# Kernel optimization log

Measured on AMD Instinct MI355X. Metric: run time of the kernel, lower is better.

The kernel has to match this reference:

```python
import jax, jax.numpy as jnp
import numpy as np

N_HEADS = 16

def setup_inputs() -> dict:
    key = jax.random.key(0)
    k1, k2, k3 = jax.random.split(key, 3)
    B, L, D = 2, 2048, 1024
    x = jax.random.normal(k1, (B, L, D), dtype=jnp.float32)
    w_qkv = jax.random.normal(k2, (D, 3 * D), dtype=jnp.float32) * (D ** -0.5)
    w_proj = jax.random.normal(k3, (D, D), dtype=jnp.float32) * (D ** -0.5)
    return {"x": x, "w_qkv": w_qkv, "w_proj": w_proj}

def reference(x, w_qkv, w_proj):
    B, L, D = x.shape
    H = N_HEADS
    dh = D // H
    qkv = x @ w_qkv  # [B,L,3D]
    q, k, v = jnp.split(qkv, 3, axis=-1)
    def heads(t):
        return t.reshape(B, L, H, dh).transpose(0, 2, 1, 3)  # [B,H,L,dh]
    q, k, v = heads(q), heads(k), heads(v)
    s = jnp.einsum('bhqd,bhkd->bhqk', q, k) / jnp.sqrt(jnp.float32(dh))
    causal = jnp.tril(jnp.ones((L, L), dtype=bool))
    s = jnp.where(causal[None, None], s, jnp.float32(-jnp.inf))
    w = jax.nn.softmax(s, axis=-1)
    o = jnp.einsum('bhqk,bhkd->bhqd', w, v)  # [B,H,L,dh]
    o = o.transpose(0, 2, 1, 3).reshape(B, L, D)
    return o @ w_proj
```

## Files before the change

kernel.cpp:

```cpp
#include <hip/hip_runtime.h>
#include <hip/hip_bf16.h>
#include <cstddef>

typedef __attribute__((ext_vector_type(8))) short bf16x8;
typedef __attribute__((ext_vector_type(4))) float f32x4;
typedef __attribute__((ext_vector_type(4))) unsigned short us4;
typedef __attribute__((ext_vector_type(8))) unsigned short us8;
typedef unsigned short u16;
typedef unsigned int u32;

__device__ __forceinline__ u16 f2bf(float f) {
    unsigned u = __builtin_bit_cast(unsigned, f);
    u += 0x7FFFu + ((u >> 16) & 1u);
    return (u16)(u >> 16);
}
__device__ __forceinline__ float bf2f(u16 h) {
    unsigned u = ((unsigned)h) << 16;
    return __builtin_bit_cast(float, u);
}

__device__ __forceinline__ void gl_lds16(const u16* g, u16* l) {
    __builtin_amdgcn_global_load_lds(
        (const __attribute__((address_space(1))) u32*)g,
        (__attribute__((address_space(3))) u32*)l, 16, 0, 0);
}

template <int N>
__device__ __forceinline__ void wait_vmcnt() {
    if constexpr (N == 8)      asm volatile("s_waitcnt vmcnt(8)" ::: "memory");
    else if constexpr (N == 6) asm volatile("s_waitcnt vmcnt(6)" ::: "memory");
    else                       asm volatile("s_waitcnt vmcnt(0)" ::: "memory");
}

__global__ __launch_bounds__(256) void split_rm(const float* __restrict__ in,
                                                u16* __restrict__ hi,
                                                u16* __restrict__ lo, int n4) {
    int i = blockIdx.x * 256 + threadIdx.x;
    const int stride = gridDim.x * 256;
    for (; i < n4; i += stride) {
        f32x4 v = ((const f32x4*)in)[i];
        us4 h, l;
#pragma unroll
        for (int e = 0; e < 4; ++e) {
            u16 hb = f2bf(v[e]);
            h[e] = hb;
            l[e] = f2bf(v[e] - bf2f(hb));
        }
        ((us4*)hi)[i] = h;
        ((us4*)lo)[i] = l;
    }
}

__global__ __launch_bounds__(256) void split_T(const float* __restrict__ in, int inRS,
                                               u16* __restrict__ oh,
                                               u16* __restrict__ ol, int outRS) {
    __shared__ u16 Th[64][68], Tl[64][68];
    const int tid = threadIdx.x;
    const int sr = tid >> 4;
    const int sc = (tid & 15) * 4;
    const size_t r0 = (size_t)blockIdx.y * 64;
    const size_t c0 = (size_t)blockIdx.x * 64;

#pragma unroll
    for (int i = 0; i < 4; ++i) {
        int r = sr + i * 16;
        f32x4 v = *(const f32x4*)(in + (r0 + r) * inRS + c0 + sc);
#pragma unroll
        for (int e = 0; e < 4; ++e) {
            u16 hb = f2bf(v[e]);
            Th[sc + e][r] = hb;
            Tl[sc + e][r] = f2bf(v[e] - bf2f(hb));
        }
    }
    __syncthreads();
#pragma unroll
    for (int i = 0; i < 4; ++i) {
        int r = sr + i * 16;
        *(us4*)&oh[(c0 + r) * outRS + r0 + sc] = *(const us4*)&Th[r][sc];
        *(us4*)&ol[(c0 + r) * outRS + r0 + sc] = *(const us4*)&Tl[r][sc];
    }
}

template <int BN>
__global__ __launch_bounds__(256, 2) void gemm_bf2(
    const u16* __restrict__ Ah_g, const u16* __restrict__ Al_g,
    const u16* __restrict__ Bh_g, const u16* __restrict__ Bl_g,
    int N, int K, int gy, int mode,
    float* __restrict__ Cf,
    u16* __restrict__ qsh, u16* __restrict__ qsl,
    u16* __restrict__ ksh, u16* __restrict__ ksl,
    float* __restrict__ vtmp) {
    constexpr int NB    = BN / 32;
    constexpr int ASZ   = 128 * 32;
    constexpr int BSZ   = BN * 32;
    constexpr int SET   = 2 * ASZ + 2 * BSZ;
    constexpr int BCALL = BN / 64;
    constexpr int NCALL = 4 + 2 * BCALL;
    __shared__ u16 LB[2 * SET];

    const int tid  = threadIdx.x;
    const int lane = tid & 63;
    const int w    = tid >> 6;

    const int nwg = gridDim.x;
    const int swz = (blockIdx.x & 7) * (nwg >> 3) + (blockIdx.x >> 3);
    const int bm = (swz % gy) * 128;
    const int bn = (swz / gy) * BN;

    const int srow = lane >> 2;
    const int c_l  = (lane & 3) ^ ((lane >> 3) & 3);

    const u16* pA[2][2];
    const u16* pB[2][BCALL];
#pragma unroll
    for (int j = 0; j < 2; ++j) {
        const size_t r = (size_t)(bm + w * 32 + j * 16 + srow);
        pA[0][j] = Ah_g + r * K + c_l * 8;
        pA[1][j] = Al_g + r * K + c_l * 8;
    }
#pragma unroll
    for (int j = 0; j < BCALL; ++j) {
        const size_t r = (size_t)(bn + w * (BN / 4) + j * 16 + srow);
        pB[0][j] = Bh_g + r * K + c_l * 8;
        pB[1][j] = Bl_g + r * K + c_l * 8;
    }

    auto stage = [&](int buf, int kt) {
        u16* s = LB + buf * SET;
        const size_t ko = (size_t)kt * 32;
#pragma unroll
        for (int p = 0; p < 2; ++p)
#pragma unroll
            for (int j = 0; j < 2; ++j)
                gl_lds16(pA[p][j] + ko, s + p * ASZ + (w * 32 + j * 16) * 32);
#pragma unroll
        for (int p = 0; p < 2; ++p)
#pragma unroll
            for (int j = 0; j < BCALL; ++j)
                gl_lds16(pB[p][j] + ko,
                         s + 2 * ASZ + p * BSZ + (w * (BN / 4) + j * 16) * 32);
    };

    const int lr = lane & 15;
    const int lg = lane >> 4;
    const int wm = (w >> 1) * 64;
    const int wn = (w & 1) * (BN / 2);
    const int fc = (lg ^ ((lr >> 1) & 3)) * 8;

    f32x4 acc[4][NB] = {};

    const int NK = K >> 5;
    stage(0, 0);
    if (NK > 1) stage(1, 1);

    for (int kt = 0; kt < NK; ++kt) {
        const int cur = kt & 1;
        if (kt + 1 < NK) wait_vmcnt<NCALL>();
        else             wait_vmcnt<0>();
        __builtin_amdgcn_s_barrier();

        const u16* s = LB + cur * SET;
        bf16x8 fah[4], fal[4], fbh[NB], fbl[NB];
#pragma unroll
        for (int m = 0; m < 4; ++m) {
            const int ro = (wm + m * 16 + lr) * 32 + fc;
            fah[m] = __builtin_bit_cast(bf16x8, *(const us8*)(s + ro));
            fal[m] = __builtin_bit_cast(bf16x8, *(const us8*)(s + ASZ + ro));
        }
#pragma unroll
        for (int n = 0; n < NB; ++n) {
            const int ro = (wn + n * 16 + lr) * 32 + fc;
            fbh[n] = __builtin_bit_cast(bf16x8, *(const us8*)(s + 2 * ASZ + ro));
            fbl[n] = __builtin_bit_cast(bf16x8, *(const us8*)(s + 2 * ASZ + BSZ + ro));
        }
#pragma unroll
        for (int m = 0; m < 4; ++m)
#pragma unroll
            for (int n = 0; n < NB; ++n) {
                acc[m][n] = __builtin_amdgcn_mfma_f32_16x16x32_bf16(fah[m], fbh[n], acc[m][n], 0, 0, 0);
                acc[m][n] = __builtin_amdgcn_mfma_f32_16x16x32_bf16(fah[m], fbl[n], acc[m][n], 0, 0, 0);
                acc[m][n] = __builtin_amdgcn_mfma_f32_16x16x32_bf16(fal[m], fbh[n], acc[m][n], 0, 0, 0);
            }

        asm volatile("s_waitcnt lgkmcnt(0)" ::: "memory");
        __builtin_amdgcn_s_barrier();
        if (kt + 2 < NK) stage(cur, kt + 2);
    }

    const int orow = bm + wm + lg * 4;
    if (mode == 0) {
        const int ocol = bn + wn + lr;
#pragma unroll
        for (int m = 0; m < 4; ++m)
#pragma unroll
            for (int r = 0; r < 4; ++r) {
                const size_t row = (size_t)(orow + m * 16 + r);
#pragma unroll
                for (int n = 0; n < NB; ++n)
                    Cf[row * N + ocol + n * 16] = acc[m][n][r];
            }
    } else {
        const int sec = bn >> 10;
        const int cbase = (bn & 1023) + wn + lr;
#pragma unroll
        for (int m = 0; m < 4; ++m)
#pragma unroll
            for (int r = 0; r < 4; ++r) {
                const size_t row = (size_t)(orow + m * 16 + r);
#pragma unroll
                for (int n = 0; n < NB; ++n) {
                    float v = acc[m][n][r];
                    const size_t idx = row * 1024 + cbase + n * 16;
                    if (sec == 0) {
                        v *= 0.125f;
                        u16 hb = f2bf(v);
                        qsh[idx] = hb;
                        qsl[idx] = f2bf(v - bf2f(hb));
                    } else if (sec == 1) {
                        u16 hb = f2bf(v);
                        ksh[idx] = hb;
                        ksl[idx] = f2bf(v - bf2f(hb));
                    } else {
                        vtmp[idx] = v;
                    }
                }
            }
    }
}

__global__ __launch_bounds__(512, 4) void attn_v2(
    const u16* __restrict__ qsh, const u16* __restrict__ qsl,
    const u16* __restrict__ ksh, const u16* __restrict__ ksl,
    const u16* __restrict__ vth, const u16* __restrict__ vtl,
    u16* __restrict__ oh, u16* __restrict__ ol) {
    __shared__ u16 KH[4096], KL[4096], VH[4096], VL[4096];
    __shared__ u16 Ph[128][72], Pl[128][72];

    const int tid  = threadIdx.x;
    const int lane = tid & 63;
    const int w    = tid >> 6;
    const int wq0  = w * 16;
    const int lr   = lane & 15;
    const int lg   = lane >> 4;

    const int bid  = blockIdx.x;
    const int half = bid >> 8;
    const int idx  = bid & 255;
    const int bh   = idx & 31;
    const int jj   = idx >> 5;
    const int qt   = half ? jj : (15 - jj);
    const int b    = bh >> 4;
    const int h    = bh & 15;
    const int NT   = 2 * qt + 2;
    const size_t tokb = (size_t)b * 2048;

    const size_t qtok = tokb + (size_t)qt * 128 + wq0 + lr;
    const u16* qph = qsh + qtok * 1024 + h * 64 + lg * 8;
    const u16* qpl = qsl + qtok * 1024 + h * 64 + lg * 8;
    bf16x8 aqh[2], aql[2];
    aqh[0] = __builtin_bit_cast(bf16x8, *(const us8*)qph);
    aqh[1] = __builtin_bit_cast(bf16x8, *(const us8*)(qph + 32));
    aql[0] = __builtin_bit_cast(bf16x8, *(const us8*)qpl);
    aql[1] = __builtin_bit_cast(bf16x8, *(const us8*)(qpl + 32));

    const int rl    = lane >> 3;
    const int rbase = w * 8;
    const int cl    = (lane & 7) ^ rl;
    const u16* kh0 = ksh + (tokb + rbase + rl) * 1024 + h * 64 + cl * 8;
    const u16* kl0 = ksl + (tokb + rbase + rl) * 1024 + h * 64 + cl * 8;
    const u16* vh0 = vth + (size_t)(h * 64 + rbase + rl) * 4096 + tokb + cl * 8;
    const u16* vl0 = vtl + (size_t)(h * 64 + rbase + rl) * 4096 + tokb + cl * 8;
    u16* ldsKH = KH + rbase * 64;
    u16* ldsKL = KL + rbase * 64;
    u16* ldsVH = VH + rbase * 64;
    u16* ldsVL = VL + rbase * 64;

    gl_lds16(kh0, ldsKH);
    gl_lds16(kl0, ldsKL);
    gl_lds16(vh0, ldsVH);
    gl_lds16(vl0, ldsVL);

    float m_i[4], l_i[4];
    f32x4 acc_o[4] = {};
#pragma unroll
    for (int r = 0; r < 4; ++r) { m_i[r] = -1e30f; l_i[r] = 0.f; }

    for (int kt = 0; kt < NT; ++kt) {
        const int koff = kt * 64 - qt * 128;
        const bool active = !(kt == NT - 1 && wq0 < 64);

        asm volatile("s_waitcnt vmcnt(2)" ::: "memory");
        __builtin_amdgcn_s_barrier();

        f32x4 accs[4] = {};
        if (active) {
#pragma unroll
            for (int ks = 0; ks < 2; ++ks) {
                bf16x8 a0 = aqh[ks], a1 = aql[ks];
#pragma unroll
                for (int n = 0; n < 4; ++n) {
                    const int row = n * 16 + lr;
                    const u16* pk = KH + row * 64 + (((ks * 4 + lg) ^ (row & 7)) << 3);
                    bf16x8 bkh = __builtin_bit_cast(bf16x8, *(const us8*)pk);
                    bf16x8 bkl = __builtin_bit_cast(bf16x8, *(const us8*)(pk + 4096));
                    accs[n] = __builtin_amdgcn_mfma_f32_16x16x32_bf16(a0, bkh, accs[n], 0, 0, 0);
                    accs[n] = __builtin_amdgcn_mfma_f32_16x16x32_bf16(a0, bkl, accs[n], 0, 0, 0);
                    accs[n] = __builtin_amdgcn_mfma_f32_16x16x32_bf16(a1, bkh, accs[n], 0, 0, 0);
                }
            }
            if (koff + 63 > wq0) {
#pragma unroll
                for (int n = 0; n < 4; ++n)
#pragma unroll
                    for (int rr = 0; rr < 4; ++rr)
                        if (koff + n * 16 + lr > wq0 + 4 * lg + rr)
                            accs[n][rr] = -1e30f;
            }
#pragma unroll
            for (int rr = 0; rr < 4; ++rr) {
                float pm = fmaxf(fmaxf(accs[0][rr], accs[1][rr]),
                                 fmaxf(accs[2][rr], accs[3][rr]));
#pragma unroll
                for (int off = 1; off < 16; off <<= 1)
                    pm = fmaxf(pm, __shfl_xor(pm, off));
                float mnew  = fmaxf(m_i[rr], pm);
                float alpha = __expf(m_i[rr] - mnew);
                float ps = 0.f;
                const int prow = wq0 + 4 * lg + rr;
#pragma unroll
                for (int n = 0; n < 4; ++n) {
                    float p = __expf(accs[n][rr] - mnew);
                    u16 phb = f2bf(p);
                    Ph[prow][n * 16 + lr] = phb;
                    Pl[prow][n * 16 + lr] = f2bf(p - bf2f(phb));
                    ps += p;
                }
#pragma unroll
                for (int off = 1; off < 16; off <<= 1)
                    ps += __shfl_xor(ps, off);
                l_i[rr] = l_i[rr] * alpha + ps;
                m_i[rr] = mnew;
#pragma unroll
                for (int n = 0; n < 4; ++n) acc_o[n][rr] *= alpha;
            }
        }

        asm volatile("s_waitcnt vmcnt(0)" ::: "memory");
        asm volatile("s_waitcnt lgkmcnt(0)" ::: "memory");
        __builtin_amdgcn_s_barrier();

        if (kt + 1 < NT) {
            gl_lds16(kh0 + (size_t)(kt + 1) * 65536, ldsKH);
            gl_lds16(kl0 + (size_t)(kt + 1) * 65536, ldsKL);
        }

        if (active) {
#pragma unroll
            for (int ks = 0; ks < 2; ++ks) {
                bf16x8 aph = __builtin_bit_cast(bf16x8, *(const us8*)&Ph[wq0 + lr][ks * 32 + lg * 8]);
                bf16x8 apl = __builtin_bit_cast(bf16x8, *(const us8*)&Pl[wq0 + lr][ks * 32 + lg * 8]);
#pragma unroll
                for (int n = 0; n < 4; ++n) {
                    const int row = n * 16 + lr;
                    const u16* pv = VH + row * 64 + (((ks * 4 + lg) ^ (row & 7)) << 3);
                    bf16x8 bvh = __builtin_bit_cast(bf16x8, *(const us8*)pv);
                    bf16x8 bvl = __builtin_bit_cast(bf16x8, *(const us8*)(pv + 4096));
                    acc_o[n] = __builtin_amdgcn_mfma_f32_16x16x32_bf16(aph, bvh, acc_o[n], 0, 0, 0);
                    acc_o[n] = __builtin_amdgcn_mfma_f32_16x16x32_bf16(aph, bvl, acc_o[n], 0, 0, 0);
                    acc_o[n] = __builtin_amdgcn_mfma_f32_16x16x32_bf16(apl, bvh, acc_o[n], 0, 0, 0);
                }
            }
        }

        asm volatile("s_waitcnt lgkmcnt(0)" ::: "memory");
        __builtin_amdgcn_s_barrier();

        if (kt + 1 < NT) {
            gl_lds16(vh0 + (kt + 1) * 64, ldsVH);
            gl_lds16(vl0 + (kt + 1) * 64, ldsVL);
        }
    }

#pragma unroll
    for (int rr = 0; rr < 4; ++rr) {
        float inv = 1.0f / l_i[rr];
        const size_t q = (size_t)qt * 128 + wq0 + 4 * lg + rr;
#pragma unroll
        for (int n = 0; n < 4; ++n) {
            float v = acc_o[n][rr] * inv;
            const size_t oidx = (tokb + q) * 1024 + h * 64 + n * 16 + lr;
            u16 hb = f2bf(v);
            oh[oidx] = hb;
            ol[oidx] = f2bf(v - bf2f(hb));
        }
    }
}

extern "C" void kernel_launch(void* const* d_in, const int* in_sizes, int n_in,
                              void* d_out, int out_size, void* d_ws, size_t ws_size,
                              hipStream_t stream) {
    const float* x      = (const float*)d_in[0];
    const float* w_qkv  = (const float*)d_in[1];
    const float* w_proj = (const float*)d_in[2];
    float* out = (float*)d_out;

    char* ws = (char*)d_ws;
    const size_t MB = 1u << 20;
    u16* wqkvT_h  = (u16*)(ws + 0 * MB);
    u16* wqkvT_l  = (u16*)(ws + 6 * MB);
    u16* wprojT_h = (u16*)(ws + 12 * MB);
    u16* wprojT_l = (u16*)(ws + 14 * MB);
    u16* xh       = (u16*)(ws + 16 * MB);
    u16* xl       = (u16*)(ws + 24 * MB);
    u16* qsh      = (u16*)(ws + 32 * MB);
    u16* qsl      = (u16*)(ws + 40 * MB);
    u16* ksh      = (u16*)(ws + 48 * MB);
    u16* ksl      = (u16*)(ws + 56 * MB);
    float* vtmp   = (float*)(ws + 64 * MB);
    u16* vth = xh;
    u16* vtl = xl;
    u16* oh = (u16*)vtmp;
    u16* ol = oh + (size_t)4096 * 1024;

    split_rm<<<2048, 256, 0, stream>>>(x, xh, xl, 4096 * 1024 / 4);
    split_T<<<dim3(48, 16), 256, 0, stream>>>(w_qkv, 3072, wqkvT_h, wqkvT_l, 1024);
    split_T<<<dim3(16, 16), 256, 0, stream>>>(w_proj, 1024, wprojT_h, wprojT_l, 1024);

    gemm_bf2<128><<<dim3(768), 256, 0, stream>>>(xh, xl, wqkvT_h, wqkvT_l,
                                                 3072, 1024, 32, 1,
                                                 nullptr, qsh, qsl, ksh, ksl, vtmp);

    split_T<<<dim3(16, 64), 256, 0, stream>>>(vtmp, 1024, vth, vtl, 4096);

    attn_v2<<<dim3(512), 512, 0, stream>>>(qsh, qsl, ksh, ksl, vth, vtl, oh, ol);

    gemm_bf2<64><<<dim3(512), 256, 0, stream>>>(oh, ol, wprojT_h, wprojT_l,
                                                1024, 1024, 32, 0,
                                                out, nullptr, nullptr, nullptr, nullptr, nullptr);
}
```

Baseline: 322.6 us.

## Fuse input split kernels, widen QKV GEMM tile, remap block swizzle

Merges the three fp32-to-bf16 hi/lo split launches (x, w_qkv, w_proj) into a single prep kernel dispatched on block index, removing two launches. The QKV GEMM moves from a 128-wide to a 192-wide N tile, cutting the grid from 768 to 512 blocks, and its epilogue now derives the Q/K/V section per column because a 192-wide tile can straddle section boundaries. Block-to-tile mapping becomes a parameterised grouped swizzle (RM/RBM/RBN) aimed at L2 reuse. The 64-wide projection GEMM gets a higher occupancy hint. The wider tile raises register and LDS pressure.

After: 296.9 us. 8.0% less time.

```diff
diff --git a/kernel.cpp b/kernel.cpp
--- a/kernel.cpp
+++ b/kernel.cpp
@@ -27,27 +27,35 @@
 
 template <int N>
 __device__ __forceinline__ void wait_vmcnt() {
-    if constexpr (N == 8)      asm volatile("s_waitcnt vmcnt(8)" ::: "memory");
+    if constexpr (N == 10)     asm volatile("s_waitcnt vmcnt(10)" ::: "memory");
+    else if constexpr (N == 8) asm volatile("s_waitcnt vmcnt(8)" ::: "memory");
     else if constexpr (N == 6) asm volatile("s_waitcnt vmcnt(6)" ::: "memory");
     else                       asm volatile("s_waitcnt vmcnt(0)" ::: "memory");
 }
 
-__global__ __launch_bounds__(256) void split_rm(const float* __restrict__ in,
-                                                u16* __restrict__ hi,
-                                                u16* __restrict__ lo, int n4) {
-    int i = blockIdx.x * 256 + threadIdx.x;
-    const int stride = gridDim.x * 256;
-    for (; i < n4; i += stride) {
-        f32x4 v = ((const f32x4*)in)[i];
-        us4 h, l;
+__device__ __forceinline__ void tsplit64(const float* __restrict__ in, int inRS,
+                                         u16* __restrict__ oh, u16* __restrict__ ol,
+                                         int outRS, size_t r0, size_t c0, int tid,
+                                         u16 (*Th)[68], u16 (*Tl)[68]) {
+    const int sr = tid >> 4;
+    const int sc = (tid & 15) * 4;
+#pragma unroll
+    for (int i = 0; i < 4; ++i) {
+        int r = sr + i * 16;
+        f32x4 v = *(const f32x4*)(in + (r0 + r) * inRS + c0 + sc);
 #pragma unroll
         for (int e = 0; e < 4; ++e) {
             u16 hb = f2bf(v[e]);
-            h[e] = hb;
-            l[e] = f2bf(v[e] - bf2f(hb));
-        }
-        ((us4*)hi)[i] = h;
-        ((us4*)lo)[i] = l;
+            Th[sc + e][r] = hb;
+            Tl[sc + e][r] = f2bf(v[e] - bf2f(hb));
+        }
+    }
+    __syncthreads();
+#pragma unroll
+    for (int i = 0; i < 4; ++i) {
+        int r = sr + i * 16;
+        *(us4*)&oh[(c0 + r) * outRS + r0 + sc] = *(const us4*)&Th[r][sc];
+        *(us4*)&ol[(c0 + r) * outRS + r0 + sc] = *(const us4*)&Tl[r][sc];
     }
 }
 
@@ -55,37 +63,50 @@
                                                u16* __restrict__ oh,
                                                u16* __restrict__ ol, int outRS) {
     __shared__ u16 Th[64][68], Tl[64][68];
+    tsplit64(in, inRS, oh, ol, outRS,
+             (size_t)blockIdx.y * 64, (size_t)blockIdx.x * 64, threadIdx.x, Th, Tl);
+}
+
+__global__ __launch_bounds__(256) void prep_fused(
+    const float* __restrict__ x, const float* __restrict__ w_qkv,
+    const float* __restrict__ w_proj,
+    u16* __restrict__ xh, u16* __restrict__ xl,
+    u16* __restrict__ wqh, u16* __restrict__ wql,
+    u16* __restrict__ wph, u16* __restrict__ wpl) {
+    __shared__ u16 Th[64][68], Tl[64][68];
+    const int bid = blockIdx.x;
     const int tid = threadIdx.x;
-    const int sr = tid >> 4;
-    const int sc = (tid & 15) * 4;
-    const size_t r0 = (size_t)blockIdx.y * 64;
-    const size_t c0 = (size_t)blockIdx.x * 64;
-
-#pragma unroll
-    for (int i = 0; i < 4; ++i) {
-        int r = sr + i * 16;
-        f32x4 v = *(const f32x4*)(in + (r0 + r) * inRS + c0 + sc);
-#pragma unroll
-        for (int e = 0; e < 4; ++e) {
-            u16 hb = f2bf(v[e]);
-            Th[sc + e][r] = hb;
-            Tl[sc + e][r] = f2bf(v[e] - bf2f(hb));
-        }
-    }
-    __syncthreads();
-#pragma unroll
-    for (int i = 0; i < 4; ++i) {
-        int r = sr + i * 16;
-        *(us4*)&oh[(c0 + r) * outRS + r0 + sc] = *(const us4*)&Th[r][sc];
-        *(us4*)&ol[(c0 + r) * outRS + r0 + sc] = *(const us4*)&Tl[r][sc];
+    if (bid < 1024) {
+        const int n4 = 4096 * 1024 / 4;
+        int i = bid * 256 + tid;
+        for (; i < n4; i += 1024 * 256) {
+            f32x4 v = ((const f32x4*)x)[i];
+            us4 h, l;
+#pragma unroll
+            for (int e = 0; e < 4; ++e) {
+                u16 hb = f2bf(v[e]);
+                h[e] = hb;
+                l[e] = f2bf(v[e] - bf2f(hb));
+            }
+            ((us4*)xh)[i] = h;
+            ((us4*)xl)[i] = l;
+        }
+    } else if (bid < 1792) {
+        const int t = bid - 1024;
+        tsplit64(w_qkv, 3072, wqh, wql, 1024,
+                 (size_t)(t / 48) * 64, (size_t)(t % 48) * 64, tid, Th, Tl);
+    } else {
+        const int t = bid - 1792;
+        tsplit64(w_proj, 1024, wph, wpl, 1024,
+                 (size_t)(t / 16) * 64, (size_t)(t % 16) * 64, tid, Th, Tl);
     }
 }
 
 template <int BN>
-__global__ __launch_bounds__(256, 2) void gemm_bf2(
+__global__ __launch_bounds__(256, BN == 64 ? 3 : 2) void gemm_bf2(
     const u16* __restrict__ Ah_g, const u16* __restrict__ Al_g,
     const u16* __restrict__ Bh_g, const u16* __restrict__ Bl_g,
-    int N, int K, int gy, int mode,
+    int N, int K, int RM, int RBM, int RBN, int mode,
     float* __restrict__ Cf,
     u16* __restrict__ qsh, u16* __restrict__ qsl,
     u16* __restrict__ ksh, u16* __restrict__ ksl,
@@ -102,10 +123,10 @@
     const int lane = tid & 63;
     const int w    = tid >> 6;
 
-    const int nwg = gridDim.x;
-    const int swz = (blockIdx.x & 7) * (nwg >> 3) + (blockIdx.x >> 3);
-    const int bm = (swz % gy) * 128;
-    const int bn = (swz / gy) * BN;
+    const int x = blockIdx.x & 7;
+    const int j = blockIdx.x >> 3;
+    const int bm = ((x % RM) * RBM + j % RBM) * 128;
+    const int bn = ((x / RM) * RBN + j / RBM) * BN;
 
     const int srow = lane >> 2;
     const int c_l  = (lane & 3) ^ ((lane >> 3) & 3);
@@ -113,16 +134,16 @@
     const u16* pA[2][2];
     const u16* pB[2][BCALL];
 #pragma unroll
-    for (int j = 0; j < 2; ++j) {
-        const size_t r = (size_t)(bm + w * 32 + j * 16 + srow);
-        pA[0][j] = Ah_g + r * K + c_l * 8;
-        pA[1][j] = Al_g + r * K + c_l * 8;
-    }
-#pragma unroll
-    for (int j = 0; j < BCALL; ++j) {
-        const size_t r = (size_t)(bn + w * (BN / 4) + j * 16 + srow);
-        pB[0][j] = Bh_g + r * K + c_l * 8;
-        pB[1][j] = Bl_g + r * K + c_l * 8;
+    for (int jj = 0; jj < 2; ++jj) {
+        const size_t r = (size_t)(bm + w * 32 + jj * 16 + srow);
+        pA[0][jj] = Ah_g + r * K + c_l * 8;
+        pA[1][jj] = Al_g + r * K + c_l * 8;
+    }
+#pragma unroll
+    for (int jj = 0; jj < BCALL; ++jj) {
+        const size_t r = (size_t)(bn + w * (BN / 4) + jj * 16 + srow);
+        pB[0][jj] = Bh_g + r * K + c_l * 8;
+        pB[1][jj] = Bl_g + r * K + c_l * 8;
     }
 
     auto stage = [&](int buf, int kt) {
@@ -131,14 +152,14 @@
 #pragma unroll
         for (int p = 0; p < 2; ++p)
 #pragma unroll
-            for (int j = 0; j < 2; ++j)
-                gl_lds16(pA[p][j] + ko, s + p * ASZ + (w * 32 + j * 16) * 32);
+            for (int jj = 0; jj < 2; ++jj)
+                gl_lds16(pA[p][jj] + ko, s + p * ASZ + (w * 32 + jj * 16) * 32);
 #pragma unroll
         for (int p = 0; p < 2; ++p)
 #pragma unroll
-            for (int j = 0; j < BCALL; ++j)
-                gl_lds16(pB[p][j] + ko,
-                         s + 2 * ASZ + p * BSZ + (w * (BN / 4) + j * 16) * 32);
+            for (int jj = 0; jj < BCALL; ++jj)
+                gl_lds16(pB[p][jj] + ko,
+                         s + 2 * ASZ + p * BSZ + (w * (BN / 4) + jj * 16) * 32);
     };
 
     const int lr = lane & 15;
@@ -200,17 +221,17 @@
                     Cf[row * N + ocol + n * 16] = acc[m][n][r];
             }
     } else {
-        const int sec = bn >> 10;
-        const int cbase = (bn & 1023) + wn + lr;
-#pragma unroll
-        for (int m = 0; m < 4; ++m)
-#pragma unroll
-            for (int r = 0; r < 4; ++r) {
-                const size_t row = (size_t)(orow + m * 16 + r);
-#pragma unroll
-                for (int n = 0; n < NB; ++n) {
+#pragma unroll
+        for (int n = 0; n < NB; ++n) {
+            const int col  = bn + wn + n * 16 + lr;
+            const int sec  = col >> 10;
+            const int cidx = col & 1023;
+#pragma unroll
+            for (int m = 0; m < 4; ++m)
+#pragma unroll
+                for (int r = 0; r < 4; ++r) {
                     float v = acc[m][n][r];
-                    const size_t idx = row * 1024 + cbase + n * 16;
+                    const size_t idx = (size_t)(orow + m * 16 + r) * 1024 + cidx;
                     if (sec == 0) {
                         v *= 0.125f;
                         u16 hb = f2bf(v);
@@ -224,7 +245,7 @@
                         vtmp[idx] = v;
                     }
                 }
-            }
+        }
     }
 }
 
@@ -422,12 +443,12 @@
     u16* oh = (u16*)vtmp;
     u16* ol = oh + (size_t)4096 * 1024;
 
-    split_rm<<<2048, 256, 0, stream>>>(x, xh, xl, 4096 * 1024 / 4);
-    split_T<<<dim3(48, 16), 256, 0, stream>>>(w_qkv, 3072, wqkvT_h, wqkvT_l, 1024);
-    split_T<<<dim3(16, 16), 256, 0, stream>>>(w_proj, 1024, wprojT_h, wprojT_l, 1024);
-
-    gemm_bf2<128><<<dim3(768), 256, 0, stream>>>(xh, xl, wqkvT_h, wqkvT_l,
-                                                 3072, 1024, 32, 1,
+    prep_fused<<<dim3(2048), 256, 0, stream>>>(x, w_qkv, w_proj,
+                                               xh, xl, wqkvT_h, wqkvT_l,
+                                               wprojT_h, wprojT_l);
+
+    gemm_bf2<192><<<dim3(512), 256, 0, stream>>>(xh, xl, wqkvT_h, wqkvT_l,
+                                                 3072, 1024, 4, 8, 8, 1,
                                                  nullptr, qsh, qsl, ksh, ksl, vtmp);
 
     split_T<<<dim3(16, 64), 256, 0, stream>>>(vtmp, 1024, vth, vtl, 4096);
@@ -435,6 +456,6 @@
     attn_v2<<<dim3(512), 512, 0, stream>>>(qsh, qsl, ksh, ksl, vth, vtl, oh, ol);
 
     gemm_bf2<64><<<dim3(512), 256, 0, stream>>>(oh, ol, wprojT_h, wprojT_l,
-                                                1024, 1024, 32, 0,
+                                                1024, 1024, 4, 8, 8, 0,
                                                 out, nullptr, nullptr, nullptr, nullptr, nullptr);
 }
```
